# Optimization experiments

Measured on AMD Instinct MI355X. Metric: run time of the kernel, lower is better.

The kernel has to match this reference:

```python
import jax, jax.numpy as jnp
import numpy as np

B_SZ, L, D, N, H = 2, 2048, 1024, 16, 128

def celu(x):
    # F.celu with alpha=1: max(0,x) + min(0, exp(x)-1)
    return jnp.where(x > 0, x, jnp.expm1(x))

def setup_inputs() -> dict:
    key = jax.random.key(0)
    ks = jax.random.split(key, 16)
    s = lambda fan_in: 1.0 / np.sqrt(fan_in)
    inp = {
        "x": jax.random.normal(ks[0], (B_SZ, L, D), jnp.float32),
        # fc1: d->d, fc2/fc3: d->n
        "W1": jax.random.normal(ks[1], (D, D), jnp.float32) * s(D),
        "b1": jnp.zeros((D,), jnp.float32),
        "W2": jax.random.normal(ks[2], (D, N), jnp.float32) * s(D),
        "b2": jnp.zeros((N,), jnp.float32),
        "W3": jax.random.normal(ks[3], (D, N), jnp.float32) * s(D),
        "b3": jnp.zeros((N,), jnp.float32),
        # lift_fn: Linear(d,128) -> relu -> Linear(128,d) -> tanh
        "Wl1": jax.random.normal(ks[4], (D, H), jnp.float32) * s(D),
        "bl1": jnp.zeros((H,), jnp.float32),
        "Wl2": jax.random.normal(ks[5], (H, D), jnp.float32) * s(H),
        "bl2": jnp.zeros((D,), jnp.float32),
        # fc_net: Linear(2d,128) -> relu -> (dropout, eval: identity) -> Linear(128,d)
        "Wf1": jax.random.normal(ks[6], (2 * D, H), jnp.float32) * s(2 * D),
        "bf1": jnp.zeros((H,), jnp.float32),
        "Wf2": jax.random.normal(ks[7], (H, D), jnp.float32) * s(H),
        "bf2": jnp.zeros((D,), jnp.float32),
        "state_init": jnp.zeros((1, D, N), jnp.float32),
        # kaiming_normal_ on (d, n): std = sqrt(2 / fan_in), fan_in = n
        "A": jax.random.normal(ks[8], (D, N), jnp.float32) * np.sqrt(2.0 / N),
    }
    return inp

def reference(x, W1, b1, W2, b2, W3, b3, Wl1, bl1, Wl2, bl2, Wf1, bf1, Wf2, bf2, state_init, A):
    b = x.shape[0]
    # lift_fn
    lifted = jnp.tanh(jax.nn.relu(x @ Wl1 + bl1) @ Wl2 + bl2)          # [b,l,d]
    combined = jnp.concatenate([x, lifted], axis=-1)                    # [b,l,2d]
    x_trans = jax.nn.relu(combined @ Wf1 + bf1) @ Wf2 + bf2             # [b,l,d]
    h_prev = jnp.broadcast_to(state_init, (b,) + state_init.shape[1:])  # [b,d,n]
    Bm = x_trans @ W2 + b2                                              # [b,l,n]
    Cm = x_trans @ W3 + b3                                              # [b,l,n]
    delta = jax.nn.softplus(x_trans @ W1 + b1)                          # [b,l,d]
    # discretization: bldn outer products
    dB = delta[..., :, None] * Bm[..., None, :]                         # [b,l,d,n]
    dA = jnp.exp(-celu(delta[..., :, None] * A[None, None]))            # [b,l,d,n]
    h_new = dA * h_prev[:, None] + x_trans[..., None] * dB              # [b,l,d,n]
    output = jnp.einsum('bln,bldn->bld', Cm, h_new)                     # [b,l,d]
    last_h_state = h_new[:, -1]                                         # [b,d,n]
    return (output, last_h_state)
```

## Files before the change

kernel.cpp:

```cpp
#include <hip/hip_runtime.h>
#include <cmath>

#define B_SZ 2
#define LSEQ 2048
#define DDIM 1024
#define NDIM 16
#define HDIM 128
#define MROWS (B_SZ * LSEQ)
#define NBIG (DDIM + 2 * NDIM)
#define NPAD 1088

typedef __bf16 bf16x8 __attribute__((ext_vector_type(8)));
typedef __bf16 bf16x4 __attribute__((ext_vector_type(4)));
typedef float f32x4 __attribute__((ext_vector_type(4)));

__device__ __forceinline__ void glds16(const __bf16* g, __bf16* l) {
    __builtin_amdgcn_global_load_lds(
        (const __attribute__((address_space(1))) unsigned int*)g,
        (__attribute__((address_space(3))) unsigned int*)l, 16, 0, 0);
}

__device__ __forceinline__ int slot_xt(int d) { return (d >> 4) * 32 + (d & 15); }
__device__ __forceinline__ int slot_de(int d) { return (d >> 4) * 32 + 16 + (d & 15); }

__device__ __forceinline__ void tcast_tile(const float* __restrict__ in,
                                           __bf16* __restrict__ out, int K, int N,
                                           int bx, int by, float (*t)[33]) {
    int tx = threadIdx.x & 31, ty = threadIdx.x >> 5;
    int n0 = bx * 32, k0 = by * 32;
    #pragma unroll
    for (int i = 0; i < 4; ++i) {
        int k = k0 + ty + i * 8, n = n0 + tx;
        t[ty + i * 8][tx] = (k < K && n < N) ? in[(size_t)k * N + n] : 0.f;
    }
    __syncthreads();
    #pragma unroll
    for (int i = 0; i < 4; ++i) {
        int n = n0 + ty + i * 8, k = k0 + tx;
        if (n < N && k < K) out[(size_t)n * K + k] = (__bf16)t[tx][ty + i * 8];
    }
}

__device__ __forceinline__ void tcast_pair_tile(const float* __restrict__ in,
                                                __bf16* __restrict__ out,
                                                int bx, int by, float (*t)[33]) {
    int tx = threadIdx.x & 31, ty = threadIdx.x >> 5;
    int n0 = bx * 32, k0 = by * 32;
    #pragma unroll
    for (int i = 0; i < 4; ++i) {
        int k = k0 + ty + i * 8, n = n0 + tx;
        t[ty + i * 8][tx] = in[(size_t)k * 1024 + n];
    }
    __syncthreads();
    #pragma unroll
    for (int i = 0; i < 4; ++i) {
        int n = n0 + ty + i * 8, k = k0 + tx;
        out[(size_t)slot_xt(n) * 128 + k] = (__bf16)t[tx][ty + i * 8];
    }
}

__global__ __launch_bounds__(256) void pack_all(
    const float* W1, const float* W2, const float* W3, const float* Wl1,
    const float* Wl2, const float* Wf1, const float* Wf2,
    const float* bf2, const float* h0,
    __bf16* WbigT, __bf16* WaT, __bf16* Wf1bT, __bf16* Wl2T, __bf16* WpairT,
    __bf16* Wf2c, float* bias_pair, unsigned* h0mask) {
    __shared__ float t[32][33];
    const int b = blockIdx.x;
    const int tid = threadIdx.x;
    if (b < 1024) {
        tcast_tile(W1, WbigT, 1024, 1024, b & 31, b >> 5, t);
    } else if (b < 1152) {
        int i = b - 1024; tcast_tile(Wl1, WaT, 1024, 128, i & 3, i >> 2, t);
    } else if (b < 1280) {
        int i = b - 1152; tcast_tile(Wf1, WaT + 128 * 1024, 1024, 128, i & 3, i >> 2, t);
    } else if (b < 1408) {
        int i = b - 1280;
        tcast_tile(Wf1 + (size_t)1024 * 128, Wf1bT, 1024, 128, i & 3, i >> 2, t);
    } else if (b < 1536) {
        int i = b - 1408; tcast_tile(Wl2, Wl2T, 128, 1024, i & 31, i >> 5, t);
    } else if (b < 1664) {
        int i = b - 1536; tcast_pair_tile(Wf2, WpairT, i & 31, i >> 5, t);
    } else if (b < 1696) {
        int i = b - 1664; tcast_tile(W2, WbigT + (size_t)1024 * 1024, 1024, 16, 0, i, t);
    } else if (b < 1728) {
        int i = b - 1696; tcast_tile(W3, WbigT + (size_t)1040 * 1024, 1024, 16, 0, i, t);
    } else if (b < 1732) {
        int i = (b - 1728) * 256 + tid;
        bias_pair[slot_xt(i)] = bf2[i];
    } else if (b < 1764) {
        int i = (b - 1732) * 256 + tid;
        #pragma unroll
        for (int r = 0; r < 4; ++r) {
            int e = i + r * 8192;
            if (e < 32 * 1024) WbigT[(size_t)1056 * 1024 + e] = (__bf16)0.f;
        }
    } else if (b < 1796) {
        int id = (b - 1764) * 256 + tid;
        #pragma unroll
        for (int j = 0; j < 4; ++j) {
            int e = id + j * 8192;
            float4 v = ((const float4*)Wf2)[e];
            bf16x4 o2 = {(__bf16)v.x, (__bf16)v.y, (__bf16)v.z, (__bf16)v.w};
            ((bf16x4*)Wf2c)[e] = o2;
        }
    } else {
        __shared__ unsigned sm[32];
        if (tid < 32) sm[tid] = 0u;
        __syncthreads();
        unsigned nib = 0;
        #pragma unroll
        for (int j = 0; j < 4; ++j) {
            int d = tid * 4 + j;
            const uint4* hu = (const uint4*)(h0 + d * NDIM);
            uint4 a0 = hu[0], a1 = hu[1], a2 = hu[2], a3 = hu[3];
            unsigned nz = a0.x | a0.y | a0.z | a0.w | a1.x | a1.y | a1.z | a1.w |
                          a2.x | a2.y | a2.z | a2.w | a3.x | a3.y | a3.z | a3.w;
            if (nz) nib |= (1u << j);
        }
        if (nib) atomicOr(&sm[(tid * 4) >> 5], nib << ((tid * 4) & 31));
        __syncthreads();
        if (tid < 32) h0mask[tid] = sm[tid];
    }
}

template <int BM, int BN, int BK, int NBUF, int ACT, bool ADD_PREV, bool GUARDN, bool AF32>
__device__ __forceinline__ void gemm_core(
    const void* Av, int lda, const __bf16* __restrict__ Bt, int ldb, int Ntot,
    const float* __restrict__ bias, const __bf16* __restrict__ prev, int ldp,
    __bf16* __restrict__ C, int ldc, int K, int bm, int bn,
    __bf16* As, __bf16* Bs) {
    constexpr int WM = BM / 2, WN = BN / 2, FM = WM / 16, FN = WN / 16;
    constexpr int ASZ = BM * BK, BSZ = BN * BK;
    constexpr int CPR = BK / 8;
    constexpr int NH = BK / 32;
    const int tid = threadIdx.x;
    const int lane = tid & 63, w = tid >> 6;
    const int wr = w >> 1, wc = w & 1;
    const int g = lane >> 4, lr = lane & 15;
    const __bf16* A16 = (const __bf16*)Av;
    const float* A32 = (const float*)Av;

    auto stage = [&](int buf, int k0) {
        #pragma unroll
        for (int i = 0; i < BM * BK / 2048; ++i) {
            int D = i * 256 + tid;
            int row = D / CPR, pos = D % CPR, c = pos ^ (row & 7);
            if constexpr (AF32) {
                const float* s = &A32[(size_t)(bm + row) * lda + k0 + c * 8];
                float4 v0 = *(const float4*)s;
                float4 v1 = *(const float4*)(s + 4);
                bf16x8 pk = {(__bf16)v0.x, (__bf16)v0.y, (__bf16)v0.z, (__bf16)v0.w,
                             (__bf16)v1.x, (__bf16)v1.y, (__bf16)v1.z, (__bf16)v1.w};
                *(bf16x8*)&As[buf * ASZ + row * BK + pos * 8] = pk;
            } else {
                glds16(&A16[(size_t)(bm + row) * lda + k0 + c * 8],
                       &As[buf * ASZ + (i * 256 + w * 64) * 8]);
            }
        }
        #pragma unroll
        for (int i = 0; i < BN * BK / 2048; ++i) {
            int D = i * 256 + tid;
            int row = D / CPR, pos = D % CPR, c = pos ^ (row & 7);
            glds16(&Bt[(size_t)(bn + row) * ldb + k0 + c * 8],
                   &Bs[buf * BSZ + (i * 256 + w * 64) * 8]);
        }
    };

    f32x4 acc[FM][FN] = {};
    const int x7 = lr & 7;
    int ca[NH];
    #pragma unroll
    for (int h = 0; h < NH; ++h) ca[h] = ((h * 4 + g) ^ x7) * 8;
    const int arow0 = wr * WM + lr;
    const int brow0 = wc * WN + lr;

    const int nt = K / BK;
    stage(0, 0);
    __syncthreads();
    for (int t = 0; t < nt; ++t) {
        if (NBUF == 2 && t + 1 < nt) stage((t + 1) & 1, (t + 1) * BK);
        const __bf16* Ab = &As[(NBUF == 2 ? (t & 1) : 0) * ASZ];
        const __bf16* Bb = &Bs[(NBUF == 2 ? (t & 1) : 0) * BSZ];
        bf16x8 af[FM][NH], bfr[FN][NH];
        #pragma unroll
        for (int m = 0; m < FM; ++m)
            #pragma unroll
            for (int h = 0; h < NH; ++h)
                af[m][h] = *(const bf16x8*)&Ab[(arow0 + m * 16) * BK + ca[h]];
        #pragma unroll
        for (int n = 0; n < FN; ++n)
            #pragma unroll
            for (int h = 0; h < NH; ++h)
                bfr[n][h] = *(const bf16x8*)&Bb[(brow0 + n * 16) * BK + ca[h]];
        #pragma unroll
        for (int h = 0; h < NH; ++h)
            #pragma unroll
            for (int m = 0; m < FM; ++m)
                #pragma unroll
                for (int n = 0; n < FN; ++n)
                    acc[m][n] = __builtin_amdgcn_mfma_f32_16x16x32_bf16(
                        af[m][h], bfr[n][h], acc[m][n], 0, 0, 0);
        __syncthreads();
    }

    #pragma unroll
    for (int m = 0; m < FM; ++m) {
        #pragma unroll
        for (int n = 0; n < FN; ++n) {
            #pragma unroll
            for (int r = 0; r < 4; ++r) {
                int grow = bm + wr * WM + m * 16 + g * 4 + r;
                int gcol = bn + wc * WN + n * 16 + lr;
                if (!GUARDN || gcol < Ntot) {
                    float v = acc[m][n][r];
                    int orow = grow;
                    if (ACT == 1) {
                        v += bias[gcol];
                        if (ADD_PREV) v += (float)prev[(size_t)grow * ldp + gcol];
                        v = fmaxf(v, 0.f);
                    } else if (ACT == 2) {
                        v += bias[gcol];
                        float e = __expf(2.f * v);
                        v = 1.f - 2.f * __builtin_amdgcn_rcpf(e + 1.f);
                    } else if (ACT == 4) {
                        if (gcol < HDIM) v = fmaxf(v + bias[gcol], 0.f);
                    } else if (ACT == 7) {
                        orow = (grow < 1024) ? slot_de(grow) : 2048 + (grow - 1024);
                    }
                    C[(size_t)orow * ldc + gcol] = (__bf16)v;
                }
            }
        }
    }
}

__global__ __launch_bounds__(256) void stage2_k(
    const float* __restrict__ x, const __bf16* __restrict__ WaT,
    const __bf16* __restrict__ WbigT, const __bf16* __restrict__ Wf2c,
    const float* __restrict__ bf2, const float* __restrict__ b1,
    const float* __restrict__ b2, const float* __restrict__ b3,
    const float* __restrict__ bl1,
    __bf16* __restrict__ tmp12, __bf16* __restrict__ WpairT,
    float* __restrict__ bias_pair) {
    __shared__ __bf16 As[8192];
    __shared__ __bf16 Bs[16384];
    const int b = blockIdx.x;
    if (b < 512) {
        const int aid = (b & 7) * 64 + (b >> 3);
        const int bn = (aid & 3) * 64, bm = (aid >> 2) * 32;
        gemm_core<32, 64, 128, 2, 4, false, false, true>(
            x, DDIM, WaT, 1024, 256, bl1, nullptr, 0, tmp12, 256, 1024, bm, bn, As, Bs);
    } else if (b < 580) {
        const int aid = b - 512;
        const int bm = (aid >> 1) * 32, bn = (aid & 1) * 64;
        gemm_core<32, 64, 128, 2, 7, false, false, false>(
            WbigT, 1024, Wf2c, 1024, 128, nullptr, nullptr, 0,
            WpairT, 128, 1024, bm, bn, As, Bs);
    } else {
        const int n = (b - 580) * 4 + (threadIdx.x >> 6);
        const int lane = threadIdx.x & 63;
        const __bf16* wr = WbigT + (size_t)n * 1024 + lane * 16;
        float s = 0.f;
        #pragma unroll
        for (int i = 0; i < 2; ++i) {
            bf16x8 wv = *(const bf16x8*)&wr[i * 8];
            float4 f0 = *(const float4*)&bf2[lane * 16 + i * 8];
            float4 f1 = *(const float4*)&bf2[lane * 16 + i * 8 + 4];
            s += (float)wv[0] * f0.x + (float)wv[1] * f0.y + (float)wv[2] * f0.z +
                 (float)wv[3] * f0.w + (float)wv[4] * f1.x + (float)wv[5] * f1.y +
                 (float)wv[6] * f1.z + (float)wv[7] * f1.w;
        }
        #pragma unroll
        for (int off = 32; off; off >>= 1) s += __shfl_down(s, off);
        if (lane == 0) {
            float base = (n < DDIM) ? b1[n]
                       : (n < DDIM + NDIM) ? b2[n - DDIM] : b3[n - DDIM - NDIM];
            int sl = (n < DDIM) ? slot_de(n) : 2048 + (n - DDIM);
            bias_pair[sl] = base + s;
        }
    }
}

__global__ __launch_bounds__(512) void g23_k(
    const __bf16* __restrict__ tmp12, const __bf16* __restrict__ Wl2T,
    const __bf16* __restrict__ Wf1bT, const float* __restrict__ bl2,
    const float* __restrict__ bf1, __bf16* __restrict__ tmp2) {
    __shared__ __bf16 T1[2048];
    __shared__ __bf16 LS[2048];
    __shared__ __bf16 B1[2][16384];
    __shared__ __bf16 B2[2][16384];
    const int tid = threadIdx.x;
    const int lane = tid & 63, w = tid >> 6;
    const int g = lane >> 4, lr = lane & 15;
    const int x7 = lr & 7;
    const int bm = blockIdx.x * 16;

    if (tid < 256) {
        int row = tid >> 4, pos = tid & 15, c = pos ^ (row & 7);
        glds16(&tmp12[(size_t)(bm + row) * 256 + c * 8], &T1[w * 512]);
    }
    auto stageB = [&](int buf, int kc) {
        #pragma unroll
        for (int i = 0; i < 4; ++i) {
            int D = i * 512 + tid;
            int row = D >> 4, pos = D & 15, c = pos ^ (row & 7);
            glds16(&Wl2T[(size_t)(kc + row) * 128 + c * 8],
                   &B1[buf][(i * 512 + w * 64) * 8]);
            glds16(&Wf1bT[(size_t)row * 1024 + kc + c * 8],
                   &B2[buf][(i * 512 + w * 64) * 8]);
        }
    };

    int ca[4];
    #pragma unroll
    for (int h = 0; h < 4; ++h) ca[h] = ((h * 4 + g) ^ x7) * 8;
    const int col = w * 16 + lr;
    const int brow = col * 128;

    stageB(0, 0);
    __syncthreads();
    bf16x8 a1[4];
    #pragma unroll
    for (int h = 0; h < 4; ++h) a1[h] = *(const bf16x8*)&T1[lr * 128 + ca[h]];

    f32x4 acc2 = {};
    for (int t = 0; t < 8; ++t) {
        if (t + 1 < 8) stageB((t + 1) & 1, (t + 1) * 128);
        const __bf16* b1b = B1[t & 1];
        const __bf16* b2b = B2[t & 1];
        f32x4 acc1 = {};
        #pragma unroll
        for (int h = 0; h < 4; ++h) {
            bf16x8 bf = *(const bf16x8*)&b1b[brow + ca[h]];
            acc1 = __builtin_amdgcn_mfma_f32_16x16x32_bf16(a1[h], bf, acc1, 0, 0, 0);
        }
        const float bl = bl2[t * 128 + col];
        const int chunk = col >> 3, cin = col & 7;
        #pragma unroll
        for (int r = 0; r < 4; ++r) {
            float v = acc1[r] + bl;
            float e = __expf(2.f * v);
            v = 1.f - 2.f * __builtin_amdgcn_rcpf(e + 1.f);
            int row = g * 4 + r;
            LS[row * 128 + ((chunk ^ (row & 7)) << 3) + cin] = (__bf16)v;
        }
        __syncthreads();
        #pragma unroll
        for (int h = 0; h < 4; ++h) {
            bf16x8 a2 = *(const bf16x8*)&LS[lr * 128 + ca[h]];
            bf16x8 bf = *(const bf16x8*)&b2b[brow + ca[h]];
            acc2 = __builtin_amdgcn_mfma_f32_16x16x32_bf16(a2, bf, acc2, 0, 0, 0);
        }
        __syncthreads();
    }

    const float bfv = bf1[col];
    #pragma unroll
    for (int r = 0; r < 4; ++r) {
        const int row = g * 4 + r;
        float v = acc2[r] + bfv + (float)tmp12[(size_t)(bm + row) * 256 + 128 + col];
        v = fmaxf(v, 0.f);
        tmp2[(size_t)(bm + row) * 128 + col] = (__bf16)v;
    }
}

__global__ __launch_bounds__(256) void mm_pairs(
    const __bf16* __restrict__ tmp2, const __bf16* __restrict__ WpairT,
    const float* __restrict__ bias_pair,
    const float* __restrict__ Amat, const float* __restrict__ h0,
    const unsigned* __restrict__ h0mask,
    float* __restrict__ out, float* __restrict__ last_h) {
    constexpr int ASZ = 128 * 64, BSZ = 64 * 64;
    __shared__ __bf16 As[2 * ASZ];
    __shared__ __bf16 Bs[2 * BSZ];
    const int NB = gridDim.x;
    const int aid = (blockIdx.x & 7) * (NB >> 3) + (blockIdx.x >> 3);
    const int bn = (aid & 31) * 64, bm = (aid >> 5) * 128;
    const int tid = threadIdx.x;
    const int lane = tid & 63, w = tid >> 6;
    const int wr = w >> 1, wc = w & 1;
    const int g = lane >> 4, lr = lane & 15;

    auto stage = [&](int buf, int k0) {
        #pragma unroll
        for (int i = 0; i < 4; ++i) {
            int D = i * 256 + tid;
            int row = D >> 3, pos = D & 7, c = pos ^ (row & 7);
            glds16(&tmp2[(size_t)(bm + row) * 128 + k0 + c * 8],
                   &As[buf * ASZ + (i * 256 + w * 64) * 8]);
        }
        #pragma unroll
        for (int i = 0; i < 2; ++i) {
            int D = i * 256 + tid;
            int row = D >> 3, pos = D & 7, c = pos ^ (row & 7);
            glds16(&WpairT[(size_t)(bn + row) * 128 + k0 + c * 8],
                   &Bs[buf * BSZ + (i * 256 + w * 64) * 8]);
        }
    };

    f32x4 acc[4][2] = {};
    const int x7 = lr & 7;
    const int ca[2] = {(g ^ x7) * 8, ((4 + g) ^ x7) * 8};
    const int arow0 = wr * 64 + lr, brow0 = wc * 32 + lr;
    stage(0, 0);
    __syncthreads();
    #pragma unroll
    for (int t = 0; t < 2; ++t) {
        if (t == 0) stage(1, 64);
        const __bf16* Ab = &As[t * ASZ];
        const __bf16* Bb = &Bs[t * BSZ];
        bf16x8 af[4][2], bfr[2][2];
        #pragma unroll
        for (int m = 0; m < 4; ++m)
            #pragma unroll
            for (int h = 0; h < 2; ++h)
                af[m][h] = *(const bf16x8*)&Ab[(arow0 + m * 16) * 64 + ca[h]];
        #pragma unroll
        for (int n = 0; n < 2; ++n)
            #pragma unroll
            for (int h = 0; h < 2; ++h)
                bfr[n][h] = *(const bf16x8*)&Bb[(brow0 + n * 16) * 64 + ca[h]];
        #pragma unroll
        for (int h = 0; h < 2; ++h)
            #pragma unroll
            for (int m = 0; m < 4; ++m)
                #pragma unroll
                for (int n = 0; n < 2; ++n)
                    acc[m][n] = __builtin_amdgcn_mfma_f32_16x16x32_bf16(
                        af[m][h], bfr[n][h], acc[m][n], 0, 0, 0);
        __syncthreads();
    }

    {
        int row = tid >> 3, pos = tid & 7, c = pos ^ (row & 7);
        #pragma unroll
        for (int t2 = 0; t2 < 2; ++t2)
            glds16(&WpairT[(size_t)(2048 + row) * 128 + t2 * 64 + c * 8],
                   &Bs[t2 * 2048 + w * 512]);
    }
    __syncthreads();
    f32x4 accB[2] = {}, accC[2] = {};
    #pragma unroll
    for (int t2 = 0; t2 < 2; ++t2) {
        const __bf16* Ab = &As[t2 * ASZ];
        #pragma unroll
        for (int h = 0; h < 2; ++h) {
            bf16x8 bB = *(const bf16x8*)&Bs[t2 * 2048 + lr * 64 + ca[h]];
            bf16x8 bC = *(const bf16x8*)&Bs[t2 * 2048 + (16 + lr) * 64 + ca[h]];
            #pragma unroll
            for (int m2 = 0; m2 < 2; ++m2) {
                bf16x8 a2 = *(const bf16x8*)&Ab[(w * 32 + m2 * 16 + lr) * 64 + ca[h]];
                accB[m2] = __builtin_amdgcn_mfma_f32_16x16x32_bf16(a2, bB, accB[m2], 0, 0, 0);
                accC[m2] = __builtin_amdgcn_mfma_f32_16x16x32_bf16(a2, bC, accC[m2], 0, 0, 0);
            }
        }
    }
    __syncthreads();
    float* sCB = (float*)As;
    __bf16* sBC = &Bs[BSZ];
    const float bB_ = bias_pair[2048 + lr], bC_ = bias_pair[2064 + lr];
    #pragma unroll
    for (int m2 = 0; m2 < 2; ++m2) {
        #pragma unroll
        for (int r = 0; r < 4; ++r) {
            int lrow = w * 32 + m2 * 16 + g * 4 + r;
            float vB = accB[m2][r] + bB_;
            float vC = accC[m2][r] + bC_;
            sBC[lrow * 32 + lr] = (__bf16)vB;
            sBC[lrow * 32 + 16 + lr] = (__bf16)vC;
            float p = vB * vC;
            #pragma unroll
            for (int m3 = 1; m3 < 16; m3 <<= 1) p += __shfl_xor(p, m3);
            if (lr == 0) sCB[lrow] = p;
        }
    }
    __syncthreads();

    const int d = ((bn + wc * 32) >> 1) + lr;
    const float bx_ = bias_pair[bn + wc * 32 + lr];
    const float bd_ = bias_pair[bn + wc * 32 + 16 + lr];
    const bool msk = (h0mask[d >> 5] >> (d & 31)) & 1u;
    #pragma unroll
    for (int m = 0; m < 4; ++m) {
        #pragma unroll
        for (int r = 0; r < 4; ++r) {
            const int lrow = wr * 64 + m * 16 + g * 4 + r;
            const int row = bm + lrow;
            const float xt = acc[m][0][r] + bx_;
            const float dr = acc[m][1][r] + bd_;
            const float e = __expf(-fabsf(dr));
            const float de = fmaxf(dr, 0.f) + __logf(1.f + e);
            const float xd = xt * de;
            float res = xd * sCB[lrow];
            const bool is_last = (row & (LSEQ - 1)) == (LSEQ - 1);
            if (msk) {
                float s = 0.f;
                #pragma unroll
                for (int n = 0; n < NDIM; ++n) {
                    float z = de * Amat[d * NDIM + n];
                    float c2 = (z > 0.f) ? z : __expf(z) - 1.f;
                    float da = __expf(-c2);
                    float h0v = h0[d * NDIM + n];
                    s += (float)sBC[lrow * 32 + 16 + n] * da * h0v;
                    if (is_last)
                        last_h[(((size_t)(row >> 11)) * DDIM + d) * NDIM + n] =
                            da * h0v + xd * (float)sBC[lrow * 32 + n];
                }
                res += s;
            } else if (is_last) {
                #pragma unroll
                for (int n = 0; n < NDIM; ++n)
                    last_h[(((size_t)(row >> 11)) * DDIM + d) * NDIM + n] =
                        xd * (float)sBC[lrow * 32 + n];
            }
            out[(size_t)row * DDIM + d] = res;
        }
    }
}

extern "C" void kernel_launch(void* const* d_in, const int* in_sizes, int n_in,
                              void* d_out, int out_size, void* d_ws, size_t ws_size,
                              hipStream_t stream) {
    const float* x   = (const float*)d_in[0];
    const float* W1  = (const float*)d_in[1];
    const float* b1  = (const float*)d_in[2];
    const float* W2  = (const float*)d_in[3];
    const float* b2  = (const float*)d_in[4];
    const float* W3  = (const float*)d_in[5];
    const float* b3  = (const float*)d_in[6];
    const float* Wl1 = (const float*)d_in[7];
    const float* bl1 = (const float*)d_in[8];
    const float* Wl2 = (const float*)d_in[9];
    const float* bl2 = (const float*)d_in[10];
    const float* Wf1 = (const float*)d_in[11];
    const float* bf1 = (const float*)d_in[12];
    const float* Wf2 = (const float*)d_in[13];
    const float* bf2 = (const float*)d_in[14];
    const float* h0  = (const float*)d_in[15];
    const float* Amat= (const float*)d_in[16];

    float* out    = (float*)d_out;
    float* last_h = (float*)d_out + (size_t)MROWS * DDIM;

    __bf16* wsb = (__bf16*)d_ws;
    size_t o = 0;
    auto alloc = [&](size_t n) { __bf16* p = wsb + o; o += n; return p; };
    __bf16* WaT    = alloc(256 * 1024);
    __bf16* Wf1bT  = alloc(128 * 1024);
    __bf16* Wl2T   = alloc(1024 * 128);
    __bf16* WbigT  = alloc((size_t)NPAD * 1024);
    __bf16* WpairT = alloc(2112 * 128);
    __bf16* Wf2c   = alloc(128 * 1024);
    __bf16* tmp12  = alloc((size_t)MROWS * 256);
    __bf16* tmp2   = alloc((size_t)MROWS * HDIM);
    float*  bias_pair = (float*)(wsb + o); o += 2 * 2112;
    unsigned* h0mask = (unsigned*)(wsb + o);

    pack_all<<<dim3(1797), 256, 0, stream>>>(W1, W2, W3, Wl1, Wl2, Wf1, Wf2,
                                             bf2, h0,
                                             WbigT, WaT, Wf1bT, Wl2T, WpairT,
                                             Wf2c, bias_pair, h0mask);
    stage2_k<<<dim3(844), 256, 0, stream>>>(x, WaT, WbigT, Wf2c, bf2, b1, b2, b3,
                                            bl1, tmp12, WpairT, bias_pair);
    g23_k<<<dim3(256), 512, 0, stream>>>(tmp12, Wl2T, Wf1bT, bl2, bf1, tmp2);
    mm_pairs<<<dim3(32 * 32), 256, 0, stream>>>(tmp2, WpairT, bias_pair,
                                                Amat, h0, h0mask, out, last_h);
}
```

Before: 51.28 us.

## Reschedule weight packing across stages to overlap with first GEMM

Moves most weight transposes and casts out of the standalone pack kernel and into the first GEMM stage, so they run as independent blocks alongside the x·[Wl1|Wf1a] GEMM. Only the WaT pack stays in a small prologue kernel. The lift/fc1 chain (old g23_k) is merged with the Wbig×Wf2 pair GEMM and the bias reduction into one 512-thread stage3 kernel, with shared memory split per half-block. Launch count stays at four, but the work per stage is rebalanced to cut serial dependency bubbles. The cost is more complex block dispatch and larger shared-memory use that may limit occupancy.

```diff
diff --git a/kernel.cpp b/kernel.cpp
--- a/kernel.cpp
+++ b/kernel.cpp
@@ -59,68 +59,14 @@
     }
 }
 
-__global__ __launch_bounds__(256) void pack_all(
-    const float* W1, const float* W2, const float* W3, const float* Wl1,
-    const float* Wl2, const float* Wf1, const float* Wf2,
-    const float* bf2, const float* h0,
-    __bf16* WbigT, __bf16* WaT, __bf16* Wf1bT, __bf16* Wl2T, __bf16* WpairT,
-    __bf16* Wf2c, float* bias_pair, unsigned* h0mask) {
+__global__ __launch_bounds__(256) void pack_wat(const float* Wl1, const float* Wf1,
+                                                __bf16* WaT) {
     __shared__ float t[32][33];
     const int b = blockIdx.x;
-    const int tid = threadIdx.x;
-    if (b < 1024) {
-        tcast_tile(W1, WbigT, 1024, 1024, b & 31, b >> 5, t);
-    } else if (b < 1152) {
-        int i = b - 1024; tcast_tile(Wl1, WaT, 1024, 128, i & 3, i >> 2, t);
-    } else if (b < 1280) {
-        int i = b - 1152; tcast_tile(Wf1, WaT + 128 * 1024, 1024, 128, i & 3, i >> 2, t);
-    } else if (b < 1408) {
-        int i = b - 1280;
-        tcast_tile(Wf1 + (size_t)1024 * 128, Wf1bT, 1024, 128, i & 3, i >> 2, t);
-    } else if (b < 1536) {
-        int i = b - 1408; tcast_tile(Wl2, Wl2T, 128, 1024, i & 31, i >> 5, t);
-    } else if (b < 1664) {
-        int i = b - 1536; tcast_pair_tile(Wf2, WpairT, i & 31, i >> 5, t);
-    } else if (b < 1696) {
-        int i = b - 1664; tcast_tile(W2, WbigT + (size_t)1024 * 1024, 1024, 16, 0, i, t);
-    } else if (b < 1728) {
-        int i = b - 1696; tcast_tile(W3, WbigT + (size_t)1040 * 1024, 1024, 16, 0, i, t);
-    } else if (b < 1732) {
-        int i = (b - 1728) * 256 + tid;
-        bias_pair[slot_xt(i)] = bf2[i];
-    } else if (b < 1764) {
-        int i = (b - 1732) * 256 + tid;
-        #pragma unroll
-        for (int r = 0; r < 4; ++r) {
-            int e = i + r * 8192;
-            if (e < 32 * 1024) WbigT[(size_t)1056 * 1024 + e] = (__bf16)0.f;
-        }
-    } else if (b < 1796) {
-        int id = (b - 1764) * 256 + tid;
-        #pragma unroll
-        for (int j = 0; j < 4; ++j) {
-            int e = id + j * 8192;
-            float4 v = ((const float4*)Wf2)[e];
-            bf16x4 o2 = {(__bf16)v.x, (__bf16)v.y, (__bf16)v.z, (__bf16)v.w};
-            ((bf16x4*)Wf2c)[e] = o2;
-        }
-    } else {
-        __shared__ unsigned sm[32];
-        if (tid < 32) sm[tid] = 0u;
-        __syncthreads();
-        unsigned nib = 0;
-        #pragma unroll
-        for (int j = 0; j < 4; ++j) {
-            int d = tid * 4 + j;
-            const uint4* hu = (const uint4*)(h0 + d * NDIM);
-            uint4 a0 = hu[0], a1 = hu[1], a2 = hu[2], a3 = hu[3];
-            unsigned nz = a0.x | a0.y | a0.z | a0.w | a1.x | a1.y | a1.z | a1.w |
-                          a2.x | a2.y | a2.z | a2.w | a3.x | a3.y | a3.z | a3.w;
-            if (nz) nib |= (1u << j);
-        }
-        if (nib) atomicOr(&sm[(tid * 4) >> 5], nib << ((tid * 4) & 31));
-        __syncthreads();
-        if (tid < 32) h0mask[tid] = sm[tid];
+    if (b < 128) tcast_tile(Wl1, WaT, 1024, 128, b & 3, b >> 2, t);
+    else {
+        int i = b - 128;
+        tcast_tile(Wf1, WaT + 128 * 1024, 1024, 128, i & 3, i >> 2, t);
     }
 }
 
@@ -129,12 +75,11 @@
     const void* Av, int lda, const __bf16* __restrict__ Bt, int ldb, int Ntot,
     const float* __restrict__ bias, const __bf16* __restrict__ prev, int ldp,
     __bf16* __restrict__ C, int ldc, int K, int bm, int bn,
-    __bf16* As, __bf16* Bs) {
+    __bf16* As, __bf16* Bs, int tid) {
     constexpr int WM = BM / 2, WN = BN / 2, FM = WM / 16, FN = WN / 16;
     constexpr int ASZ = BM * BK, BSZ = BN * BK;
     constexpr int CPR = BK / 8;
     constexpr int NH = BK / 32;
-    const int tid = threadIdx.x;
     const int lane = tid & 63, w = tid >> 6;
     const int wr = w >> 1, wc = w & 1;
     const int g = lane >> 4, lr = lane & 15;
@@ -235,31 +180,177 @@
     }
 }
 
-__global__ __launch_bounds__(256) void stage2_k(
+__global__ __launch_bounds__(256) void stage1_k(
     const float* __restrict__ x, const __bf16* __restrict__ WaT,
-    const __bf16* __restrict__ WbigT, const __bf16* __restrict__ Wf2c,
-    const float* __restrict__ bf2, const float* __restrict__ b1,
-    const float* __restrict__ b2, const float* __restrict__ b3,
+    const float* W1, const float* W2, const float* W3, const float* Wl2,
+    const float* Wf1, const float* Wf2, const float* bf2, const float* h0,
     const float* __restrict__ bl1,
-    __bf16* __restrict__ tmp12, __bf16* __restrict__ WpairT,
-    float* __restrict__ bias_pair) {
+    __bf16* __restrict__ tmp12, __bf16* WbigT, __bf16* Wf1bT, __bf16* Wl2T,
+    __bf16* WpairT, __bf16* Wf2c, float* bias_pair, unsigned* h0mask) {
     __shared__ __bf16 As[8192];
     __shared__ __bf16 Bs[16384];
+    __shared__ float t[32][33];
     const int b = blockIdx.x;
+    const int tid = threadIdx.x;
     if (b < 512) {
         const int aid = (b & 7) * 64 + (b >> 3);
         const int bn = (aid & 3) * 64, bm = (aid >> 2) * 32;
         gemm_core<32, 64, 128, 2, 4, false, false, true>(
-            x, DDIM, WaT, 1024, 256, bl1, nullptr, 0, tmp12, 256, 1024, bm, bn, As, Bs);
-    } else if (b < 580) {
-        const int aid = b - 512;
+            x, DDIM, WaT, 1024, 256, bl1, nullptr, 0, tmp12, 256, 1024, bm, bn,
+            As, Bs, tid);
+    } else if (b < 1536) {
+        int i = b - 512; tcast_tile(W1, WbigT, 1024, 1024, i & 31, i >> 5, t);
+    } else if (b < 1664) {
+        int i = b - 1536;
+        tcast_tile(Wf1 + (size_t)1024 * 128, Wf1bT, 1024, 128, i & 3, i >> 2, t);
+    } else if (b < 1792) {
+        int i = b - 1664; tcast_tile(Wl2, Wl2T, 128, 1024, i & 31, i >> 5, t);
+    } else if (b < 1920) {
+        int i = b - 1792; tcast_pair_tile(Wf2, WpairT, i & 31, i >> 5, t);
+    } else if (b < 1952) {
+        int i = b - 1920; tcast_tile(W2, WbigT + (size_t)1024 * 1024, 1024, 16, 0, i, t);
+    } else if (b < 1984) {
+        int i = b - 1952; tcast_tile(W3, WbigT + (size_t)1040 * 1024, 1024, 16, 0, i, t);
+    } else if (b < 1988) {
+        int i = (b - 1984) * 256 + tid;
+        bias_pair[slot_xt(i)] = bf2[i];
+    } else if (b < 2020) {
+        int i = (b - 1988) * 256 + tid;
+        #pragma unroll
+        for (int r = 0; r < 4; ++r) {
+            int e = i + r * 8192;
+            if (e < 32 * 1024) WbigT[(size_t)1056 * 1024 + e] = (__bf16)0.f;
+        }
+    } else if (b < 2052) {
+        int id = (b - 2020) * 256 + tid;
+        #pragma unroll
+        for (int j = 0; j < 4; ++j) {
+            int e = id + j * 8192;
+            float4 v = ((const float4*)Wf2)[e];
+            bf16x4 o2 = {(__bf16)v.x, (__bf16)v.y, (__bf16)v.z, (__bf16)v.w};
+            ((bf16x4*)Wf2c)[e] = o2;
+        }
+    } else {
+        __shared__ unsigned sm[32];
+        if (tid < 32) sm[tid] = 0u;
+        __syncthreads();
+        unsigned nib = 0;
+        #pragma unroll
+        for (int j = 0; j < 4; ++j) {
+            int d = tid * 4 + j;
+            const uint4* hu = (const uint4*)(h0 + d * NDIM);
+            uint4 a0 = hu[0], a1 = hu[1], a2 = hu[2], a3 = hu[3];
+            unsigned nz = a0.x | a0.y | a0.z | a0.w | a1.x | a1.y | a1.z | a1.w |
+                          a2.x | a2.y | a2.z | a2.w | a3.x | a3.y | a3.z | a3.w;
+            if (nz) nib |= (1u << j);
+        }
+        if (nib) atomicOr(&sm[(tid * 4) >> 5], nib << ((tid * 4) & 31));
+        __syncthreads();
+        if (tid < 32) h0mask[tid] = sm[tid];
+    }
+}
+
+__global__ __launch_bounds__(512) void stage3_k(
+    const __bf16* __restrict__ tmp12, const __bf16* __restrict__ Wl2T,
+    const __bf16* __restrict__ Wf1bT, const __bf16* __restrict__ WbigT,
+    const __bf16* __restrict__ Wf2c,
+    const float* __restrict__ bl2, const float* __restrict__ bf1,
+    const float* __restrict__ bf2, const float* __restrict__ b1,
+    const float* __restrict__ b2, const float* __restrict__ b3,
+    __bf16* __restrict__ tmp2, __bf16* __restrict__ WpairT,
+    float* __restrict__ bias_pair) {
+    __shared__ __bf16 smem[69632];
+    const int b = blockIdx.x;
+    const int tid = threadIdx.x;
+    if (b < 256) {
+        __bf16* T1 = smem;
+        __bf16* LS = smem + 2048;
+        __bf16* B1 = smem + 4096;
+        __bf16* B2 = smem + 36864;
+        const int lane = tid & 63, w = tid >> 6;
+        const int g = lane >> 4, lr = lane & 15;
+        const int x7 = lr & 7;
+        const int bm = b * 16;
+
+        if (tid < 256) {
+            int row = tid >> 4, pos = tid & 15, c = pos ^ (row & 7);
+            glds16(&tmp12[(size_t)(bm + row) * 256 + c * 8], &T1[w * 512]);
+        }
+        auto stageB = [&](int buf, int kc) {
+            #pragma unroll
+            for (int i = 0; i < 4; ++i) {
+                int D = i * 512 + tid;
+                int row = D >> 4, pos = D & 15, c = pos ^ (row & 7);
+                glds16(&Wl2T[(size_t)(kc + row) * 128 + c * 8],
+                       &B1[buf * 16384 + (i * 512 + w * 64) * 8]);
+                glds16(&Wf1bT[(size_t)row * 1024 + kc + c * 8],
+                       &B2[buf * 16384 + (i * 512 + w * 64) * 8]);
+            }
+        };
+
+        int ca[4];
+        #pragma unroll
+        for (int h = 0; h < 4; ++h) ca[h] = ((h * 4 + g) ^ x7) * 8;
+        const int col = w * 16 + lr;
+        const int brow = col * 128;
+
+        stageB(0, 0);
+        __syncthreads();
+        bf16x8 a1[4];
+        #pragma unroll
+        for (int h = 0; h < 4; ++h) a1[h] = *(const bf16x8*)&T1[lr * 128 + ca[h]];
+
+        f32x4 acc2 = {};
+        for (int t = 0; t < 8; ++t) {
+            if (t + 1 < 8) stageB((t + 1) & 1, (t + 1) * 128);
+            const __bf16* b1b = &B1[(t & 1) * 16384];
+            const __bf16* b2b = &B2[(t & 1) * 16384];
+            f32x4 acc1 = {};
+            #pragma unroll
+            for (int h = 0; h < 4; ++h) {
+                bf16x8 bf = *(const bf16x8*)&b1b[brow + ca[h]];
+                acc1 = __builtin_amdgcn_mfma_f32_16x16x32_bf16(a1[h], bf, acc1, 0, 0, 0);
+            }
+            const float bl = bl2[t * 128 + col];
+            const int chunk = col >> 3, cin = col & 7;
+            #pragma unroll
+            for (int r = 0; r < 4; ++r) {
+                float v = acc1[r] + bl;
+                float e = __expf(2.f * v);
+                v = 1.f - 2.f * __builtin_amdgcn_rcpf(e + 1.f);
+                int row = g * 4 + r;
+                LS[row * 128 + ((chunk ^ (row & 7)) << 3) + cin] = (__bf16)v;
+            }
+            __syncthreads();
+            #pragma unroll
+            for (int h = 0; h < 4; ++h) {
+                bf16x8 a2 = *(const bf16x8*)&LS[lr * 128 + ca[h]];
+                bf16x8 bf = *(const bf16x8*)&b2b[brow + ca[h]];
+                acc2 = __builtin_amdgcn_mfma_f32_16x16x32_bf16(a2, bf, acc2, 0, 0, 0);
+            }
+            __syncthreads();
+        }
+
+        const float bfv = bf1[col];
+        #pragma unroll
+        for (int r = 0; r < 4; ++r) {
+            const int row = g * 4 + r;
+            float v = acc2[r] + bfv + (float)tmp12[(size_t)(bm + row) * 256 + 128 + col];
+            v = fmaxf(v, 0.f);
+            tmp2[(size_t)(bm + row) * 128 + col] = (__bf16)v;
+        }
+    } else if (b < 290) {
+        const int half = tid >> 8, tidh = tid & 255;
+        const int aid = (b - 256) * 2 + half;
         const int bm = (aid >> 1) * 32, bn = (aid & 1) * 64;
+        __bf16* Ah = smem + half * 24576;
+        __bf16* Bh = Ah + 8192;
         gemm_core<32, 64, 128, 2, 7, false, false, false>(
             WbigT, 1024, Wf2c, 1024, 128, nullptr, nullptr, 0,
-            WpairT, 128, 1024, bm, bn, As, Bs);
+            WpairT, 128, 1024, bm, bn, Ah, Bh, tidh);
     } else {
-        const int n = (b - 580) * 4 + (threadIdx.x >> 6);
-        const int lane = threadIdx.x & 63;
+        const int n = (b - 290) * 8 + (tid >> 6);
+        const int lane = tid & 63;
         const __bf16* wr = WbigT + (size_t)n * 1024 + lane * 16;
         float s = 0.f;
         #pragma unroll
@@ -279,89 +370,6 @@
             int sl = (n < DDIM) ? slot_de(n) : 2048 + (n - DDIM);
             bias_pair[sl] = base + s;
         }
-    }
-}
-
-__global__ __launch_bounds__(512) void g23_k(
-    const __bf16* __restrict__ tmp12, const __bf16* __restrict__ Wl2T,
-    const __bf16* __restrict__ Wf1bT, const float* __restrict__ bl2,
-    const float* __restrict__ bf1, __bf16* __restrict__ tmp2) {
-    __shared__ __bf16 T1[2048];
-    __shared__ __bf16 LS[2048];
-    __shared__ __bf16 B1[2][16384];
-    __shared__ __bf16 B2[2][16384];
-    const int tid = threadIdx.x;
-    const int lane = tid & 63, w = tid >> 6;
-    const int g = lane >> 4, lr = lane & 15;
-    const int x7 = lr & 7;
-    const int bm = blockIdx.x * 16;
-
-    if (tid < 256) {
-        int row = tid >> 4, pos = tid & 15, c = pos ^ (row & 7);
-        glds16(&tmp12[(size_t)(bm + row) * 256 + c * 8], &T1[w * 512]);
-    }
-    auto stageB = [&](int buf, int kc) {
-        #pragma unroll
-        for (int i = 0; i < 4; ++i) {
-            int D = i * 512 + tid;
-            int row = D >> 4, pos = D & 15, c = pos ^ (row & 7);
-            glds16(&Wl2T[(size_t)(kc + row) * 128 + c * 8],
-                   &B1[buf][(i * 512 + w * 64) * 8]);
-            glds16(&Wf1bT[(size_t)row * 1024 + kc + c * 8],
-                   &B2[buf][(i * 512 + w * 64) * 8]);
-        }
-    };
-
-    int ca[4];
-    #pragma unroll
-    for (int h = 0; h < 4; ++h) ca[h] = ((h * 4 + g) ^ x7) * 8;
-    const int col = w * 16 + lr;
-    const int brow = col * 128;
-
-    stageB(0, 0);
-    __syncthreads();
-    bf16x8 a1[4];
-    #pragma unroll
-    for (int h = 0; h < 4; ++h) a1[h] = *(const bf16x8*)&T1[lr * 128 + ca[h]];
-
-    f32x4 acc2 = {};
-    for (int t = 0; t < 8; ++t) {
-        if (t + 1 < 8) stageB((t + 1) & 1, (t + 1) * 128);
-        const __bf16* b1b = B1[t & 1];
-        const __bf16* b2b = B2[t & 1];
-        f32x4 acc1 = {};
-        #pragma unroll
-        for (int h = 0; h < 4; ++h) {
-            bf16x8 bf = *(const bf16x8*)&b1b[brow + ca[h]];
-            acc1 = __builtin_amdgcn_mfma_f32_16x16x32_bf16(a1[h], bf, acc1, 0, 0, 0);
-        }
-        const float bl = bl2[t * 128 + col];
-        const int chunk = col >> 3, cin = col & 7;
-        #pragma unroll
-        for (int r = 0; r < 4; ++r) {
-            float v = acc1[r] + bl;
-            float e = __expf(2.f * v);
-            v = 1.f - 2.f * __builtin_amdgcn_rcpf(e + 1.f);
-            int row = g * 4 + r;
-            LS[row * 128 + ((chunk ^ (row & 7)) << 3) + cin] = (__bf16)v;
-        }
-        __syncthreads();
-        #pragma unroll
-        for (int h = 0; h < 4; ++h) {
-            bf16x8 a2 = *(const bf16x8*)&LS[lr * 128 + ca[h]];
-            bf16x8 bf = *(const bf16x8*)&b2b[brow + ca[h]];
-            acc2 = __builtin_amdgcn_mfma_f32_16x16x32_bf16(a2, bf, acc2, 0, 0, 0);
-        }
-        __syncthreads();
-    }
-
-    const float bfv = bf1[col];
-    #pragma unroll
-    for (int r = 0; r < 4; ++r) {
-        const int row = g * 4 + r;
-        float v = acc2[r] + bfv + (float)tmp12[(size_t)(bm + row) * 256 + 128 + col];
-        v = fmaxf(v, 0.f);
-        tmp2[(size_t)(bm + row) * 128 + col] = (__bf16)v;
     }
 }
 
@@ -557,13 +565,13 @@
     float*  bias_pair = (float*)(wsb + o); o += 2 * 2112;
     unsigned* h0mask = (unsigned*)(wsb + o);
 
-    pack_all<<<dim3(1797), 256, 0, stream>>>(W1, W2, W3, Wl1, Wl2, Wf1, Wf2,
-                                             bf2, h0,
-                                             WbigT, WaT, Wf1bT, Wl2T, WpairT,
-                                             Wf2c, bias_pair, h0mask);
-    stage2_k<<<dim3(844), 256, 0, stream>>>(x, WaT, WbigT, Wf2c, bf2, b1, b2, b3,
-                                            bl1, tmp12, WpairT, bias_pair);
-    g23_k<<<dim3(256), 512, 0, stream>>>(tmp12, Wl2T, Wf1bT, bl2, bf1, tmp2);
+    pack_wat<<<dim3(256), 256, 0, stream>>>(Wl1, Wf1, WaT);
+    stage1_k<<<dim3(2053), 256, 0, stream>>>(x, WaT, W1, W2, W3, Wl2, Wf1, Wf2,
+                                             bf2, h0, bl1, tmp12, WbigT, Wf1bT,
+                                             Wl2T, WpairT, Wf2c, bias_pair, h0mask);
+    stage3_k<<<dim3(422), 512, 0, stream>>>(tmp12, Wl2T, Wf1bT, WbigT, Wf2c,
+                                            bl2, bf1, bf2, b1, b2, b3,
+                                            tmp2, WpairT, bias_pair);
     mm_pairs<<<dim3(32 * 32), 256, 0, stream>>>(tmp2, WpairT, bias_pair,
                                                 Amat, h0, h0mask, out, last_h);
 }
```

Result: slower. 58.27 us (+13.6%).
